# Optimization experiments

Hardware: AMD Instinct MI355X
Metric: run time of the kernel (lower is better)

Reference implementation:

```python
import jax, jax.numpy as jnp
import numpy as np

H, DH, L, G = 4, 16, 6, 256


def _ln(x, eps=1e-6):
    m = x.mean(-1, keepdims=True)
    v = ((x - m) ** 2).mean(-1, keepdims=True)
    return (x - m) * jax.lax.rsqrt(v + eps)


def _sh(u):
    # real spherical harmonics l=0,1,2, 'component' normalization (e3nn style), unit input
    x, y, z = u[:, 0], u[:, 1], u[:, 2]
    s3, s15, s5 = 3.0 ** 0.5, 15.0 ** 0.5, 5.0 ** 0.5
    return jnp.stack([
        jnp.ones_like(x),
        s3 * x, s3 * y, s3 * z,
        s15 * x * y, s15 * y * z, (s5 / 2.0) * (3.0 * z * z - 1.0),
        s15 * x * z, (s15 / 2.0) * (x * x - y * y),
    ], axis=-1)


def _seg_softmax(logits, seg, n):
    m = jax.ops.segment_max(logits, seg, num_segments=n)
    ex = jnp.exp(logits - m[seg])
    s = jax.ops.segment_sum(ex, seg, num_segments=n)
    return ex / (s[seg] + 1e-9)


def setup_inputs() -> dict:
    key = jax.random.key(0)
    ks = jax.random.split(key, 24)
    N, E = 16384, 262144
    D = H * DH  # 64

    def w(k, shape, fan_in):
        return (jax.random.normal(k, shape, dtype=jnp.float32) / np.sqrt(fan_in)).astype(jnp.float32)

    inp = {
        'node_num': N,
        'edge_src': jax.random.randint(ks[0], (E,), 0, N, dtype=jnp.int32),
        'edge_dst': jax.random.randint(ks[1], (E,), 0, N, dtype=jnp.int32),
        'edge_vec': jax.random.normal(ks[2], (E, 3), dtype=jnp.float32) * 2.0,
        'batch': jnp.sort(jax.random.randint(ks[3], (N,), 0, G, dtype=jnp.int32)),
        'node_atom': jax.random.randint(ks[4], (N,), 0, 120, dtype=jnp.int32),
        'ele_embed_w': jax.random.normal(ks[5], (120, 32), dtype=jnp.float32) * 0.05,
        'W_embed': w(ks[6], (32, D), 32),
        'W_edge': w(ks[7], (32 + 32 + 9 + 64, D), 137),
        'Wq': w(ks[8], (L, D, D), D),
        'Wk': w(ks[9], (L, D, D), D),
        'Wv': w(ks[10], (L, D, D), D),
        'Wr1': w(ks[11], (L, 64, 64), 64),
        'Wr2': w(ks[12], (L, 64, H), 64),
        'Wo': w(ks[13], (L, D, D), D),
        'W1': w(ks[14], (L, D, 4 * D), D),
        'W2': w(ks[15], (L, 4 * D, D), 4 * D),
        'W_feat': w(ks[16], (D, 512), D),
        'hW1': w(ks[17], (512, 64), 512),
        'hb1': jnp.zeros((64,), jnp.float32),
        'hW2': w(ks[18], (64, 64), 64),
        'hb2': jnp.zeros((64,), jnp.float32),
        'hW3': w(ks[19], (64, 1), 64),
        'hb3': jnp.zeros((1,), jnp.float32),
    }
    return inp


def reference(node_num, edge_src, edge_dst, edge_vec, batch, node_atom,
              ele_embed_w, W_embed, W_edge, Wq, Wk, Wv, Wr1, Wr2, Wo, W1, W2,
              W_feat, hW1, hb1, hW2, hb2, hW3, hb3):
    N = int(node_num)
    E = edge_src.shape[0]

    # edge geometry: SH of permuted+normalized edge vector, gaussian RBF of length
    r = jnp.linalg.norm(edge_vec, axis=1)
    u = edge_vec[:, jnp.array([1, 2, 0])] / (r[:, None] + 1e-12)
    sh = _sh(u)                                   # [E, 9]
    centers = jnp.linspace(0.0, 10.0, 64, dtype=jnp.float32)
    width = 0.5 * 10.0 / 64.0
    rbf = jnp.exp(-((r[:, None] - centers) ** 2) / (2.0 * width * width))  # [E, 64]
    mask = r < 10.0                               # range_dis = [0, 10)

    # w2v path: atom embedding, edge features = cat(src, dst)
    nf = ele_embed_w[node_atom]                   # [N, 32]
    x = nf @ W_embed                              # [N, 64]
    e_ctx = jnp.concatenate([nf[edge_src], nf[edge_dst], sh, rbf], axis=-1)  # [E,137]
    e = e_ctx @ W_edge                            # [E, 64]

    for l in range(L):
        h = _ln(x)
        q = (h[edge_dst] @ Wq[l]).reshape(E, H, DH)
        src_in = h[edge_src] + e
        k = (src_in @ Wk[l]).reshape(E, H, DH)
        v = (src_in @ Wv[l]).reshape(E, H, DH)
        radial = jax.nn.silu(rbf @ Wr1[l]) @ Wr2[l]           # [E, H]
        logits = (q * k).sum(-1) / np.sqrt(DH) + radial        # [E, H]
        logits = jnp.where(mask[:, None], logits, -1e9)
        alpha = _seg_softmax(logits, edge_dst, N)              # softmax over in-edges
        msg = (alpha[..., None] * v).reshape(E, H * DH)
        agg = jax.ops.segment_sum(msg, edge_dst, num_segments=N)
        x = x + agg @ Wo[l]
        h2 = _ln(x)
        x = x + jax.nn.silu(h2 @ W1[l]) @ W2[l]

    feat = _ln(x @ W_feat)                        # [N, 512], irreps_feature = 512x0e
    hh = jax.nn.relu(_ln(feat @ hW1 + hb1))
    hh = jax.nn.relu(_ln(hh @ hW2 + hb2))
    energy = hh @ hW3 + hb3                       # [N, 1]
    pooled = jax.ops.segment_sum(energy, batch, num_segments=G) / np.sqrt(72.0)
    return pooled
```

## Files before the change

### kernel.cpp

```cpp
#include <hip/hip_runtime.h>

typedef short s8v __attribute__((ext_vector_type(8)));
typedef float f32x4 __attribute__((ext_vector_type(4)));
typedef unsigned short u16;

__device__ __forceinline__ float bf2f(u16 h){
  union { unsigned u; float f; } v; v.u = ((unsigned)h) << 16; return v.f;
}
__device__ __forceinline__ u16 f2bf(float f){
  union { float f; unsigned u; } v; v.f = f;
  unsigned u = v.u;
  return (u16)((u + 0x7fffu + ((u >> 16) & 1u)) >> 16);
}
#define MFMA(a,b,c) __builtin_amdgcn_mfma_f32_16x16x32_bf16((a),(b),(c),0,0,0)

#define WREDUCE64(s) { s += __shfl_xor(s,1); s += __shfl_xor(s,2); s += __shfl_xor(s,4); \
                       s += __shfl_xor(s,8); s += __shfl_xor(s,16); s += __shfl_xor(s,32); }
#define QREDUCE16(s) { s += __shfl_xor(s,1); s += __shfl_xor(s,2); s += __shfl_xor(s,4); s += __shfl_xor(s,8); }

__device__ __forceinline__ float quad_butterfly16(float* val, int c){
  float v8[8], v4[4], v2[2];
  #pragma unroll
  for(int t=0;t<8;t++){
    float sent = (c&1) ? val[2*t] : val[2*t+1];
    float got = __shfl_xor(sent, 1);
    v8[t] = ((c&1) ? val[2*t+1] : val[2*t]) + got;
  }
  #pragma unroll
  for(int t=0;t<4;t++){
    float sent = ((c>>1)&1) ? v8[2*t] : v8[2*t+1];
    float got = __shfl_xor(sent, 2);
    v4[t] = (((c>>1)&1) ? v8[2*t+1] : v8[2*t]) + got;
  }
  #pragma unroll
  for(int t=0;t<2;t++){
    float sent = ((c>>2)&1) ? v4[2*t] : v4[2*t+1];
    float got = __shfl_xor(sent, 4);
    v2[t] = (((c>>2)&1) ? v4[2*t+1] : v4[2*t]) + got;
  }
  float sent = ((c>>3)&1) ? v2[0] : v2[1];
  float got = __shfl_xor(sent, 8);
  return (((c>>3)&1) ? v2[1] : v2[0]) + got;
}

__global__ __launch_bounds__(256) void k_prep(const float* ele, const float* W_embed, const float* W_edge,
    const float* Wq, const float* Wk, const float* Wv, const float* Wr1, const float* Wo,
    const float* W1, const float* W2, const float* W_feat, const float* hW1, const float* hW2,
    u16* dst){
  int idx = blockIdx.x*256 + threadIdx.x;
  if(idx >= 405248) return;
  u16 v;
  if(idx < 3840){
    v = f2bf(ele[idx]);
  } else if(idx < 5888){
    int l = idx - 3840;
    int cI = l >> 5, rI = l & 31;
    v = f2bf(W_embed[rI*64 + cI]);
  } else if(idx < 16128){
    int l = idx - 5888;
    int cI = l / 160, rI = l - cI*160;
    v = (rI < 137) ? f2bf(W_edge[rI*64 + cI]) : (u16)0;
  } else if(idx < 139008){
    int l = idx - 16128;
    int which = l / 24576;
    int rem = l - which*24576;
    const float* src = (which==0)?Wq:(which==1)?Wk:(which==2)?Wv:(which==3)?Wr1:Wo;
    int b = rem >> 12;
    int r2 = rem & 4095;
    int cI = r2 >> 6, rI = r2 & 63;
    v = f2bf(src[b*4096 + rI*64 + cI]);
  } else if(idx < 237312){
    int l = idx - 139008;
    int b = l / 16384;
    int rem = l - b*16384;
    int cI = rem >> 6, rI = rem & 63;
    v = f2bf(W1[b*16384 + rI*256 + cI]);
  } else if(idx < 335616){
    int l = idx - 237312;
    int b = l / 16384;
    int rem = l - b*16384;
    int cI = rem >> 8, rI = rem & 255;
    v = f2bf(W2[b*16384 + rI*64 + cI]);
  } else if(idx < 368384){
    int l = idx - 335616;
    int cI = l >> 6, rI = l & 63;
    v = f2bf(W_feat[rI*512 + cI]);
  } else if(idx < 401152){
    int l = idx - 368384;
    int cI = l >> 9, rI = l & 511;
    v = f2bf(hW1[rI*64 + cI]);
  } else {
    int l = idx - 401152;
    int cI = l >> 6, rI = l & 63;
    v = f2bf(hW2[rI*64 + cI]);
  }
  dst[idx] = v;
}

__global__ __launch_bounds__(256) void k_count(const int* dstI, int* deg, int E){
  int tid = blockIdx.x*256 + threadIdx.x;
  if(tid < E) atomicAdd(&deg[dstI[tid]], 1);
}
__global__ __launch_bounds__(1024) void k_scan(const int* deg, int* rowptr, int* cursor, int N){
  __shared__ int wsum[17];
  int tid = threadIdx.x;
  int per = (N + 1023) >> 10;
  int base = tid * per;
  int s = 0;
  for(int i=0;i<per;i++){ int idx = base+i; if(idx < N) s += deg[idx]; }
  int lane = tid & 63, wid = tid >> 6;
  int inc = s;
  for(int d=1; d<64; d<<=1){
    int t = __shfl_up(inc, d);
    if(lane >= d) inc += t;
  }
  if(lane == 63) wsum[wid+1] = inc;
  if(tid == 0) wsum[0] = 0;
  __syncthreads();
  if(tid == 0){ for(int w=1; w<=16; w++) wsum[w] += wsum[w-1]; }
  __syncthreads();
  int run = inc - s + wsum[wid];
  for(int i=0;i<per;i++){
    int idx = base + i;
    if(idx < N){ rowptr[idx] = run; cursor[idx] = run; run += deg[idx]; }
  }
  if(tid == 1023) rowptr[N] = wsum[16];
}
__global__ __launch_bounds__(256) void k_scatter(const int* dstI, int* cursor, int* csr, int E){
  int tid = blockIdx.x*256 + threadIdx.x;
  if(tid < E){
    int p = atomicAdd(&cursor[dstI[tid]], 1);
    csr[p] = tid;
  }
}

__global__ __launch_bounds__(256) void k_edge_embed(const int* csr, const int* srcI, const int* dstI,
    const int* atom, const u16* ele, const float* evec, const u16* Bt,
    u16* ebf, float* r2, int* src2, int* dst2, int E){
  int wave = (blockIdx.x*blockDim.x + threadIdx.x) >> 6;
  int lane = threadIdx.x & 63;
  int row0 = wave*16; if(row0 >= E) return;
  int c = lane & 15, q = lane >> 4;
  int p = row0 + c;
  int e = csr[p];
  int sn = srcI[e], dn = dstI[e];
  float vx = evec[(size_t)e*3+0];
  float vy = evec[(size_t)e*3+1];
  float vz = evec[(size_t)e*3+2];
  float r = sqrtf(vx*vx + vy*vy + vz*vz);
  if(q == 0){ r2[p] = r; src2[p] = sn; dst2[p] = dn; }
  float inv = 1.f/(r + 1e-12f);
  float x = vy*inv, y = vz*inv, z = vx*inv;
  const float s3 = 1.7320508075688772f, s15 = 3.872983346207417f;
  const float s5h = 1.118033988749895f, s15h = 1.9364916731037085f;
  float sh[9];
  sh[0] = 1.f; sh[1] = s3*x; sh[2] = s3*y; sh[3] = s3*z;
  sh[4] = s15*x*y; sh[5] = s15*y*z; sh[6] = s5h*(3.f*z*z - 1.f);
  sh[7] = s15*x*z; sh[8] = s15h*(x*x - y*y);
  s8v a[5];
  a[0] = *reinterpret_cast<const s8v*>(ele + (size_t)atom[sn]*32 + q*8);
  a[1] = *reinterpret_cast<const s8v*>(ele + (size_t)atom[dn]*32 + q*8);
  #pragma unroll
  for(int j=0;j<8;j++){
    int col = 64 + q*8 + j;
    u16 v;
    if(q == 0)            v = f2bf(sh[j]);
    else if(col < 73)     v = f2bf(sh[8]);
    else { float d = r - (10.f/63.f)*(float)(col-73); v = f2bf(__expf(-81.92f*d*d)); }
    a[2][j] = (short)v;
  }
  #pragma unroll
  for(int j=0;j<8;j++){
    float d = r - (10.f/63.f)*(float)(23 + q*8 + j);
    a[3][j] = (short)f2bf(__expf(-81.92f*d*d));
  }
  #pragma unroll
  for(int j=0;j<8;j++){
    int col = 128 + q*8 + j;
    u16 v = 0;
    if(col < 137){ float d = r - (10.f/63.f)*(float)(col-73); v = f2bf(__expf(-81.92f*d*d)); }
    a[4][j] = (short)v;
  }
  #pragma unroll
  for(int ct=0; ct<4; ct++){
    f32x4 acc = {0.f,0.f,0.f,0.f};
    #pragma unroll
    for(int kc=0; kc<5; kc++){
      s8v b = *reinterpret_cast<const s8v*>(Bt + (ct*16+c)*160 + kc*32 + q*8);
      acc = MFMA(a[kc], b, acc);
    }
    #pragma unroll
    for(int r_=0;r_<4;r_++) ebf[(size_t)(row0+q*4+r_)*64 + ct*16 + c] = f2bf(acc[r_]);
  }
}

__global__ __launch_bounds__(256) void k_radial6(const float* r2, const u16* Wr1T, const float* Wr2,
    float* rad6, int E){
  int wave = (blockIdx.x*256 + threadIdx.x) >> 6;
  int lane = threadIdx.x & 63;
  int row0 = wave*16; if(row0 >= E) return;
  int c = lane & 15, q = lane >> 4;
  float re = r2[row0 + c];
  s8v r0, r1;
  #pragma unroll
  for(int j=0;j<8;j++){
    float d0 = re - (10.f/63.f)*(float)(q*8+j);
    float d1 = re - (10.f/63.f)*(float)(32+q*8+j);
    r0[j] = (short)f2bf(__expf(-81.92f*d0*d0));
    r1[j] = (short)f2bf(__expf(-81.92f*d1*d1));
  }
  for(int l=0; l<6; l++){
    const u16* W1l = Wr1T + l*4096;
    const float4* wr2v = reinterpret_cast<const float4*>(Wr2 + l*256);
    float val[16];
    #pragma unroll
    for(int i=0;i<16;i++) val[i] = 0.f;
    #pragma unroll
    for(int ct=0; ct<4; ct++){
      s8v bw0 = *reinterpret_cast<const s8v*>(W1l + (ct*16+c)*64 + q*8);
      s8v bw1 = *reinterpret_cast<const s8v*>(W1l + (ct*16+c)*64 + 32 + q*8);
      f32x4 hacc = {0.f,0.f,0.f,0.f};
      hacc = MFMA(r0, bw0, hacc); hacc = MFMA(r1, bw1, hacc);
      float4 w2 = wr2v[ct*16 + c];
      #pragma unroll
      for(int r=0;r<4;r++){
        float y = hacc[r];
        float sv = y / (1.f + __expf(-y));
        val[r*4+0] += sv * w2.x;
        val[r*4+1] += sv * w2.y;
        val[r*4+2] += sv * w2.z;
        val[r*4+3] += sv * w2.w;
      }
    }
    float fin = quad_butterfly16(val, c);
    rad6[(size_t)l*E*4 + (size_t)row0*4 + lane] = fin;
  }
}

__global__ __launch_bounds__(256) void k_pre(const int* atom, const u16* ele, const u16* WembT,
    const u16* WqT0, float* xb, u16* hbf, float* Qt, int M){
  __shared__ u16 ldsH[4][16*72];
  int widL = threadIdx.x >> 6;
  int wave = (blockIdx.x*256 + threadIdx.x) >> 6;
  int lane = threadIdx.x & 63;
  int row0 = wave*16; if(row0 >= M) return;
  int c = lane & 15, q = lane >> 4;
  u16* LH = ldsH[widL];
  int at = atom[row0 + c];
  s8v a = *reinterpret_cast<const s8v*>(ele + (size_t)at*32 + q*8);
  float nx[4][4];
  #pragma unroll
  for(int ct=0; ct<4; ct++){
    s8v b = *reinterpret_cast<const s8v*>(WembT + (ct*16+c)*32 + q*8);
    f32x4 acc = {0.f,0.f,0.f,0.f};
    acc = MFMA(a, b, acc);
    #pragma unroll
    for(int r=0;r<4;r++){
      xb[(size_t)(row0+q*4+r)*64 + ct*16 + c] = acc[r];
      nx[ct][r] = acc[r];
    }
  }
  #pragma unroll
  for(int r=0;r<4;r++){
    float s = nx[0][r]+nx[1][r]+nx[2][r]+nx[3][r];
    QREDUCE16(s);
    float m = s*(1.f/64.f);
    float vv = 0.f;
    #pragma unroll
    for(int ct=0;ct<4;ct++){ float d = nx[ct][r]-m; vv += d*d; }
    QREDUCE16(vv);
    float rs = rsqrtf(vv*(1.f/64.f) + 1e-6f);
    #pragma unroll
    for(int ct=0;ct<4;ct++){
      u16 hb = f2bf((nx[ct][r]-m)*rs);
      hbf[(size_t)(row0+q*4+r)*64 + ct*16 + c] = hb;
      LH[(q*4+r)*72 + ct*16 + c] = hb;
    }
  }
  s8v h0 = *reinterpret_cast<const s8v*>(LH + c*72 + q*8);
  s8v h1 = *reinterpret_cast<const s8v*>(LH + c*72 + 32 + q*8);
  #pragma unroll
  for(int ct=0; ct<4; ct++){
    s8v b0 = *reinterpret_cast<const s8v*>(WqT0 + (ct*16+c)*64 + q*8);
    s8v b1 = *reinterpret_cast<const s8v*>(WqT0 + (ct*16+c)*64 + 32 + q*8);
    f32x4 acc = {0.f,0.f,0.f,0.f};
    acc = MFMA(h0, b0, acc);
    acc = MFMA(h1, b1, acc);
    #pragma unroll
    for(int r=0;r<4;r++) Qt[(size_t)(row0+q*4+r)*64 + c*4 + ct] = acc[r];
  }
}

__global__ __launch_bounds__(256) void k_kvrad(const u16* hbf, const u16* ebf,
    const int* src2, const int* dst2, const float* Qt, const float* r2, const float* radial,
    const u16* WkT, const u16* WvT, u16* vbf, float* exb, int E){
  int wave = (blockIdx.x*256 + threadIdx.x) >> 6;
  int lane = threadIdx.x & 63;
  int row0 = wave*16;
  int c = lane & 15, q = lane >> 4;
  int sr = src2[row0 + c];
  s8v a0, a1;
  {
    s8v h0 = *reinterpret_cast<const s8v*>(hbf + (size_t)sr*64 + q*8);
    s8v h1 = *reinterpret_cast<const s8v*>(hbf + (size_t)sr*64 + 32 + q*8);
    s8v e0 = *reinterpret_cast<const s8v*>(ebf + (size_t)(row0+c)*64 + q*8);
    s8v e1 = *reinterpret_cast<const s8v*>(ebf + (size_t)(row0+c)*64 + 32 + q*8);
    #pragma unroll
    for(int j=0;j<8;j++){
      a0[j] = (short)f2bf(bf2f((u16)h0[j]) + bf2f((u16)e0[j]));
      a1[j] = (short)f2bf(bf2f((u16)h1[j]) + bf2f((u16)e1[j]));
    }
  }
  const float4* QtV = reinterpret_cast<const float4*>(Qt);
  float4 qv[4];
  #pragma unroll
  for(int r=0;r<4;r++){
    int dr = dst2[row0 + q*4 + r];
    qv[r] = QtV[(size_t)dr*16 + c];
  }
  float val[16];
  #pragma unroll
  for(int i=0;i<16;i++) val[i] = 0.f;
  #pragma unroll
  for(int ct=0; ct<4; ct++){
    s8v bk0 = *reinterpret_cast<const s8v*>(WkT + (ct*16+c)*64 + q*8);
    s8v bk1 = *reinterpret_cast<const s8v*>(WkT + (ct*16+c)*64 + 32 + q*8);
    s8v bv0 = *reinterpret_cast<const s8v*>(WvT + (ct*16+c)*64 + q*8);
    s8v bv1 = *reinterpret_cast<const s8v*>(WvT + (ct*16+c)*64 + 32 + q*8);
    f32x4 kacc = {0.f,0.f,0.f,0.f};
    kacc = MFMA(a0, bk0, kacc); kacc = MFMA(a1, bk1, kacc);
    f32x4 vacc = {0.f,0.f,0.f,0.f};
    vacc = MFMA(a0, bv0, vacc); vacc = MFMA(a1, bv1, vacc);
    #pragma unroll
    for(int r=0;r<4;r++){
      vbf[(size_t)row0*64 + (r*4+ct)*64 + q*16 + c] = f2bf(vacc[r]);
      float qc = (ct==0)?qv[r].x:(ct==1)?qv[r].y:(ct==2)?qv[r].z:qv[r].w;
      val[r*4+ct] += 0.25f * kacc[r] * qc;
    }
  }
  float qk = quad_butterfly16(val, c);
  float logit = qk + radial[(size_t)row0*4 + lane];
  int row = row0 + q*4 + (c>>2);
  exb[(size_t)row0*4 + lane] = (r2[row] < 10.f) ? __expf(logit) : 0.f;
}

__global__ __launch_bounds__(256) void k_agg(const int* rowptr, const float* exb, const u16* vbf, u16* aggbf, int N){
  int wave = (blockIdx.x*256 + threadIdx.x) >> 6;
  int lane = threadIdx.x & 63;
  if(wave >= N) return;
  int s0 = rowptr[wave], s1 = rowptr[wave+1];
  float s[4] = {0.f,0.f,0.f,0.f};
  for(int p = s0 + lane; p < s1; p += 64){
    float4 ev = *reinterpret_cast<const float4*>(exb + (size_t)p*4);
    s[0] += ev.x; s[1] += ev.y; s[2] += ev.z; s[3] += ev.w;
  }
  #pragma unroll
  for(int i=0;i<4;i++){ WREDUCE64(s[i]); }
  int ep = lane >> 4, cc = lane & 15;
  int hh = cc >> 2;
  int swz = hh*64 + (cc&3)*4;
  float inv = 1.f/(s[hh] + 1e-9f);
  float a0=0.f, a1=0.f, a2=0.f, a3=0.f;
  for(int p = s0 + ep; p < s1; p += 4){
    int t = p & 15;
    size_t base = (size_t)(p & ~15)*64 + (size_t)((t&3)*256) + (size_t)((t>>2)*16) + swz;
    ushort4 v4 = *reinterpret_cast<const ushort4*>(vbf + base);
    float ex = exb[(size_t)p*4 + hh];
    a0 += ex*bf2f(v4.x); a1 += ex*bf2f(v4.y); a2 += ex*bf2f(v4.z); a3 += ex*bf2f(v4.w);
  }
  a0 += __shfl_xor(a0,16); a0 += __shfl_xor(a0,32);
  a1 += __shfl_xor(a1,16); a1 += __shfl_xor(a1,32);
  a2 += __shfl_xor(a2,16); a2 += __shfl_xor(a2,32);
  a3 += __shfl_xor(a3,16); a3 += __shfl_xor(a3,32);
  if(ep == 0){
    ushort4 o;
    o.x = f2bf(a0*inv); o.y = f2bf(a1*inv); o.z = f2bf(a2*inv); o.w = f2bf(a3*inv);
    *reinterpret_cast<ushort4*>(aggbf + (size_t)wave*64 + cc*4) = o;
  }
}

__global__ __launch_bounds__(256) void k_mega(const u16* aggbf, const u16* WoT, float* x,
    const u16* W1T, const u16* W2T, const u16* WqTn, float* Qt, u16* hbf, u16* xbf,
    int writex, int haveQ, int M){
  __shared__ u16 ldsH[4][16*72];
  __shared__ u16 ldsT[4][16*264];
  int widL = threadIdx.x >> 6;
  int wave = (blockIdx.x*256 + threadIdx.x) >> 6;
  int lane = threadIdx.x & 63;
  int row0 = wave*16; if(row0 >= M) return;
  int c = lane & 15, q = lane >> 4;
  u16* LH = ldsH[widL];
  u16* LT = ldsT[widL];
  {
    s8v a0 = *reinterpret_cast<const s8v*>(aggbf + (size_t)(row0+c)*64 + q*8);
    s8v a1 = *reinterpret_cast<const s8v*>(aggbf + (size_t)(row0+c)*64 + 32 + q*8);
    float nx[4][4];
    #pragma unroll
    for(int ct=0; ct<4; ct++){
      s8v b0 = *reinterpret_cast<const s8v*>(WoT + (ct*16+c)*64 + q*8);
      s8v b1 = *reinterpret_cast<const s8v*>(WoT + (ct*16+c)*64 + 32 + q*8);
      f32x4 acc = {0.f,0.f,0.f,0.f};
      acc = MFMA(a0, b0, acc);
      acc = MFMA(a1, b1, acc);
      #pragma unroll
      for(int r=0;r<4;r++){
        size_t idx = (size_t)(row0+q*4+r)*64 + ct*16 + c;
        float t = x[idx] + acc[r];
        x[idx] = t;
        nx[ct][r] = t;
      }
    }
    #pragma unroll
    for(int r=0;r<4;r++){
      float s = nx[0][r]+nx[1][r]+nx[2][r]+nx[3][r];
      QREDUCE16(s);
      float m = s*(1.f/64.f);
      float vv = 0.f;
      #pragma unroll
      for(int ct=0;ct<4;ct++){ float d = nx[ct][r]-m; vv += d*d; }
      QREDUCE16(vv);
      float rs = rsqrtf(vv*(1.f/64.f) + 1e-6f);
      #pragma unroll
      for(int ct=0;ct<4;ct++)
        LH[(q*4+r)*72 + ct*16 + c] = f2bf((nx[ct][r]-m)*rs);
    }
  }
  {
    s8v h0 = *reinterpret_cast<const s8v*>(LH + c*72 + q*8);
    s8v h1 = *reinterpret_cast<const s8v*>(LH + c*72 + 32 + q*8);
    #pragma unroll
    for(int ct=0; ct<16; ct++){
      s8v b0 = *reinterpret_cast<const s8v*>(W1T + (ct*16+c)*64 + q*8);
      s8v b1 = *reinterpret_cast<const s8v*>(W1T + (ct*16+c)*64 + 32 + q*8);
      f32x4 acc = {0.f,0.f,0.f,0.f};
      acc = MFMA(h0, b0, acc);
      acc = MFMA(h1, b1, acc);
      #pragma unroll
      for(int r=0;r<4;r++){
        float y = acc[r];
        LT[(q*4+r)*264 + ct*16 + c] = f2bf(y / (1.f + __expf(-y)));
      }
    }
  }
  {
    s8v a[8];
    #pragma unroll
    for(int kc=0; kc<8; kc++)
      a[kc] = *reinterpret_cast<const s8v*>(LT + c*264 + kc*32 + q*8);
    float nx[4][4];
    #pragma unroll
    for(int ct=0; ct<4; ct++){
      f32x4 acc = {0.f,0.f,0.f,0.f};
      #pragma unroll
      for(int kc=0; kc<8; kc++){
        s8v b = *reinterpret_cast<const s8v*>(W2T + (ct*16+c)*256 + kc*32 + q*8);
        acc = MFMA(a[kc], b, acc);
      }
      #pragma unroll
      for(int r=0;r<4;r++){
        size_t idx = (size_t)(row0+q*4+r)*64 + ct*16 + c;
        float t = x[idx] + acc[r];
        x[idx] = t;
        nx[ct][r] = t;
        if(writex) xbf[idx] = f2bf(t);
      }
    }
    #pragma unroll
    for(int r=0;r<4;r++){
      float s = nx[0][r]+nx[1][r]+nx[2][r]+nx[3][r];
      QREDUCE16(s);
      float m = s*(1.f/64.f);
      float vv = 0.f;
      #pragma unroll
      for(int ct=0;ct<4;ct++){ float d = nx[ct][r]-m; vv += d*d; }
      QREDUCE16(vv);
      float rs = rsqrtf(vv*(1.f/64.f) + 1e-6f);
      #pragma unroll
      for(int ct=0;ct<4;ct++){
        u16 hb = f2bf((nx[ct][r]-m)*rs);
        hbf[(size_t)(row0+q*4+r)*64 + ct*16 + c] = hb;
        LH[(q*4+r)*72 + ct*16 + c] = hb;
      }
    }
  }
  if(haveQ){
    s8v h0 = *reinterpret_cast<const s8v*>(LH + c*72 + q*8);
    s8v h1 = *reinterpret_cast<const s8v*>(LH + c*72 + 32 + q*8);
    #pragma unroll
    for(int ct=0; ct<4; ct++){
      s8v b0 = *reinterpret_cast<const s8v*>(WqTn + (ct*16+c)*64 + q*8);
      s8v b1 = *reinterpret_cast<const s8v*>(WqTn + (ct*16+c)*64 + 32 + q*8);
      f32x4 acc = {0.f,0.f,0.f,0.f};
      acc = MFMA(h0, b0, acc);
      acc = MFMA(h1, b1, acc);
      #pragma unroll
      for(int r=0;r<4;r++) Qt[(size_t)(row0+q*4+r)*64 + c*4 + ct] = acc[r];
    }
  }
}

__global__ __launch_bounds__(256) void k_feat_ln(const u16* A, const u16* Bt, u16* out, int M){
  int wave = (blockIdx.x*256 + threadIdx.x) >> 6;
  int lane = threadIdx.x & 63;
  int row0 = wave*16; if(row0 >= M) return;
  int c = lane & 15, q = lane >> 4;
  s8v a0 = *reinterpret_cast<const s8v*>(A + (size_t)(row0+c)*64 + q*8);
  s8v a1 = *reinterpret_cast<const s8v*>(A + (size_t)(row0+c)*64 + 32 + q*8);
  float fa[32][4];
  #pragma unroll
  for(int ct=0; ct<32; ct++){
    s8v b0 = *reinterpret_cast<const s8v*>(Bt + (ct*16+c)*64 + q*8);
    s8v b1 = *reinterpret_cast<const s8v*>(Bt + (ct*16+c)*64 + 32 + q*8);
    f32x4 acc = {0.f,0.f,0.f,0.f};
    acc = MFMA(a0, b0, acc);
    acc = MFMA(a1, b1, acc);
    #pragma unroll
    for(int r=0;r<4;r++) fa[ct][r] = acc[r];
  }
  #pragma unroll
  for(int r=0;r<4;r++){
    float s = 0.f;
    #pragma unroll
    for(int ct=0;ct<32;ct++) s += fa[ct][r];
    QREDUCE16(s);
    float m = s*(1.f/512.f);
    float vv = 0.f;
    #pragma unroll
    for(int ct=0;ct<32;ct++){ float d = fa[ct][r]-m; vv += d*d; }
    QREDUCE16(vv);
    float rs = rsqrtf(vv*(1.f/512.f) + 1e-6f);
    #pragma unroll
    for(int ct=0;ct<32;ct++)
      out[(size_t)(row0+q*4+r)*512 + ct*16 + c] = f2bf((fa[ct][r]-m)*rs);
  }
}

__global__ __launch_bounds__(256) void k_head1_ln(const u16* A, const u16* Bt, const float* hb, u16* out, int M){
  int wave = (blockIdx.x*256 + threadIdx.x) >> 6;
  int lane = threadIdx.x & 63;
  int row0 = wave*16; if(row0 >= M) return;
  int c = lane & 15, q = lane >> 4;
  s8v a[16];
  #pragma unroll
  for(int kc=0; kc<16; kc++)
    a[kc] = *reinterpret_cast<const s8v*>(A + (size_t)(row0+c)*512 + kc*32 + q*8);
  float y[4][4];
  #pragma unroll
  for(int ct=0; ct<4; ct++){
    f32x4 acc = {0.f,0.f,0.f,0.f};
    #pragma unroll
    for(int kc=0; kc<16; kc++){
      s8v b = *reinterpret_cast<const s8v*>(Bt + (size_t)(ct*16+c)*512 + kc*32 + q*8);
      acc = MFMA(a[kc], b, acc);
    }
    float bi = hb[ct*16+c];
    #pragma unroll
    for(int r=0;r<4;r++) y[ct][r] = acc[r] + bi;
  }
  #pragma unroll
  for(int r=0;r<4;r++){
    float s = y[0][r]+y[1][r]+y[2][r]+y[3][r];
    QREDUCE16(s);
    float m = s*(1.f/64.f);
    float vv = 0.f;
    #pragma unroll
    for(int ct=0;ct<4;ct++){ float d = y[ct][r]-m; vv += d*d; }
    QREDUCE16(vv);
    float rs = rsqrtf(vv*(1.f/64.f) + 1e-6f);
    #pragma unroll
    for(int ct=0;ct<4;ct++)
      out[(size_t)(row0+q*4+r)*64 + ct*16 + c] = f2bf(fmaxf((y[ct][r]-m)*rs, 0.f));
  }
}

__global__ __launch_bounds__(256) void k_head2_energy(const u16* A, const u16* Bt, const float* hb,
    const float* hW3, const float* hb3, const int* batch, float* pooled, int M){
  int wave = (blockIdx.x*256 + threadIdx.x) >> 6;
  int lane = threadIdx.x & 63;
  int row0 = wave*16; if(row0 >= M) return;
  int c = lane & 15, q = lane >> 4;
  s8v a0 = *reinterpret_cast<const s8v*>(A + (size_t)(row0+c)*64 + q*8);
  s8v a1 = *reinterpret_cast<const s8v*>(A + (size_t)(row0+c)*64 + 32 + q*8);
  float y[4][4];
  #pragma unroll
  for(int ct=0; ct<4; ct++){
    s8v b0 = *reinterpret_cast<const s8v*>(Bt + (ct*16+c)*64 + q*8);
    s8v b1 = *reinterpret_cast<const s8v*>(Bt + (ct*16+c)*64 + 32 + q*8);
    f32x4 acc = {0.f,0.f,0.f,0.f};
    acc = MFMA(a0, b0, acc);
    acc = MFMA(a1, b1, acc);
    float bi = hb[ct*16+c];
    #pragma unroll
    for(int r=0;r<4;r++) y[ct][r] = acc[r] + bi;
  }
  float w3[4];
  #pragma unroll
  for(int ct=0;ct<4;ct++) w3[ct] = hW3[ct*16+c];
  float ep[4];
  #pragma unroll
  for(int r=0;r<4;r++){
    float s = y[0][r]+y[1][r]+y[2][r]+y[3][r];
    QREDUCE16(s);
    float m = s*(1.f/64.f);
    float vv = 0.f;
    #pragma unroll
    for(int ct=0;ct<4;ct++){ float d = y[ct][r]-m; vv += d*d; }
    QREDUCE16(vv);
    float rs = rsqrtf(vv*(1.f/64.f) + 1e-6f);
    float e = 0.f;
    #pragma unroll
    for(int ct=0;ct<4;ct++) e += fmaxf((y[ct][r]-m)*rs, 0.f) * w3[ct];
    QREDUCE16(e);
    ep[r] = e;
  }
  if(c < 4){
    float ev = (c==0)?ep[0]:(c==1)?ep[1]:(c==2)?ep[2]:ep[3];
    int row = row0 + q*4 + c;
    atomicAdd(&pooled[batch[row]], ev + hb3[0]);
  }
}

__global__ __launch_bounds__(256) void k_out(const float* pooled, float* out, int G){
  int tid = blockIdx.x*256 + threadIdx.x;
  if(tid < G) out[tid] = pooled[tid] * 0.11785113019775793f;
}

extern "C" void kernel_launch(void* const* d_in, const int* in_sizes, int n_in,
                              void* d_out, int out_size, void* d_ws, size_t ws_size,
                              hipStream_t stream){
  const int*   edge_src  = (const int*)d_in[1];
  const int*   edge_dst  = (const int*)d_in[2];
  const float* edge_vec  = (const float*)d_in[3];
  const int*   batch     = (const int*)d_in[4];
  const int*   node_atom = (const int*)d_in[5];
  const float* ele    = (const float*)d_in[6];
  const float* W_embed= (const float*)d_in[7];
  const float* W_edge = (const float*)d_in[8];
  const float* Wq = (const float*)d_in[9];
  const float* Wk = (const float*)d_in[10];
  const float* Wv = (const float*)d_in[11];
  const float* Wr1= (const float*)d_in[12];
  const float* Wr2= (const float*)d_in[13];
  const float* Wo = (const float*)d_in[14];
  const float* W1 = (const float*)d_in[15];
  const float* W2 = (const float*)d_in[16];
  const float* W_feat=(const float*)d_in[17];
  const float* hW1= (const float*)d_in[18];
  const float* hb1= (const float*)d_in[19];
  const float* hW2= (const float*)d_in[20];
  const float* hb2= (const float*)d_in[21];
  const float* hW3= (const float*)d_in[22];
  const float* hb3= (const float*)d_in[23];
  (void)n_in; (void)ws_size;

  const int E = in_sizes[1];
  const int N = in_sizes[4];
  const int G = out_size;

  char* base = (char*)d_ws;
  size_t off = 0;
  #define ALLOC(ty, name, count) ty* name = (ty*)(base + off); off = (off + (size_t)(count)*sizeof(ty) + 255) & ~(size_t)255;
  ALLOC(float, r2,    E)
  ALLOC(int,   src2,  E)
  ALLOC(int,   dst2,  E)
  ALLOC(u16,   ebf,   (size_t)E*64)
  ALLOC(u16,   vbf,   (size_t)E*64)
  ALLOC(float, exb,   (size_t)E*4)
  ALLOC(float, rad6,  (size_t)E*4*6)
  ALLOC(u16,   hbf,   (size_t)N*64)
  ALLOC(u16,   aggbf, (size_t)N*64)
  ALLOC(u16,   xbf,   (size_t)N*64)
  ALLOC(float, Qt,    (size_t)N*64)
  ALLOC(float, xb,    (size_t)N*64)
  ALLOC(int,   deg,   N)
  ALLOC(int,   rowptr,N+1)
  ALLOC(int,   cursor,N)
  ALLOC(int,   csr,   E)
  ALLOC(float, pooled,G)
  ALLOC(u16, ele_bf, 120*32)
  ALLOC(u16, WembT, 64*32)
  ALLOC(u16, WedgeT,64*160)
  ALLOC(u16, WqT,  6*64*64)
  ALLOC(u16, WkT,  6*64*64)
  ALLOC(u16, WvT,  6*64*64)
  ALLOC(u16, Wr1T, 6*64*64)
  ALLOC(u16, WoT,  6*64*64)
  ALLOC(u16, W1T,  6*256*64)
  ALLOC(u16, W2T,  6*64*256)
  ALLOC(u16, WfT,  512*64)
  ALLOC(u16, hW1T, 64*512)
  ALLOC(u16, hW2T, 64*64)
  #undef ALLOC
  u16* featbf = ebf;
  u16* hh1    = (u16*)exb;

  auto cdiv = [](int a, int b){ return (a + b - 1)/b; };

  k_prep<<<cdiv(405248,256),256,0,stream>>>(ele, W_embed, W_edge, Wq, Wk, Wv, Wr1, Wo,
                                            W1, W2, W_feat, hW1, hW2, ele_bf);

  hipMemsetAsync(deg, 0, (size_t)N*sizeof(int), stream);
  hipMemsetAsync(pooled, 0, (size_t)G*sizeof(float), stream);

  k_count<<<cdiv(E,256),256,0,stream>>>(edge_dst, deg, E);
  k_scan<<<1,1024,0,stream>>>(deg, rowptr, cursor, N);
  k_scatter<<<cdiv(E,256),256,0,stream>>>(edge_dst, cursor, csr, E);
  k_edge_embed<<<E/64, 256, 0, stream>>>(csr, edge_src, edge_dst, node_atom, ele_bf, edge_vec,
                                         WedgeT, ebf, r2, src2, dst2, E);
  k_radial6<<<E/64,256,0,stream>>>(r2, Wr1T, Wr2, rad6, E);
  k_pre<<<N/64,256,0,stream>>>(node_atom, ele_bf, WembT, WqT, xb, hbf, Qt, N);

  for(int l=0; l<6; l++){
    k_kvrad<<<E/64,256,0,stream>>>(hbf, ebf, src2, dst2, Qt, r2, rad6 + (size_t)l*E*4,
                                   WkT + l*4096, WvT + l*4096, vbf, exb, E);
    k_agg<<<cdiv(N,4),256,0,stream>>>(rowptr, exb, vbf, aggbf, N);
    k_mega<<<N/64,256,0,stream>>>(aggbf, WoT + l*4096, xb,
                                  W1T + l*16384, W2T + l*16384,
                                  WqT + ((l<5)?(l+1):0)*4096, Qt, hbf, xbf,
                                  (l==5)?1:0, (l<5)?1:0, N);
  }

  k_feat_ln<<<N/64,256,0,stream>>>(xbf, WfT, featbf, N);
  k_head1_ln<<<N/64,256,0,stream>>>(featbf, hW1T, hb1, hh1, N);
  k_head2_energy<<<N/64,256,0,stream>>>(hh1, hW2T, hb2, hW3, hb3, batch, pooled, N);
  k_out<<<cdiv(G,256),256,0,stream>>>(pooled, (float*)d_out, G);
}
```

Measured before the change: 816.0 us.

## Replace per-edge radial MLP with interpolated lookup table over distance

The radial MLP depends only on the edge distance, so it is tabulated once per layer on a fine uniform grid over [0,10]. k_kvrad then linearly interpolates from the table instead of reading a precomputed per-edge, per-layer radial array. This removes the large rad6 buffer writes and reads and the per-edge MFMA work, at the cost of a small interpolation error. Block barriers are also added in the MLP kernel around shared-memory reuse.

```diff
diff --git a/kernel.cpp b/kernel.cpp
--- a/kernel.cpp
+++ b/kernel.cpp
@@ -194,13 +194,14 @@
   }
 }
 
-__global__ __launch_bounds__(256) void k_radial6(const float* r2, const u16* Wr1T, const float* Wr2,
-    float* rad6, int E){
+#define RG 4096
+#define RGROWS 4112
+__global__ __launch_bounds__(256) void k_radtab(const u16* Wr1T, const float* Wr2, float* radtab){
   int wave = (blockIdx.x*256 + threadIdx.x) >> 6;
   int lane = threadIdx.x & 63;
-  int row0 = wave*16; if(row0 >= E) return;
+  int row0 = wave*16; if(row0 >= RGROWS) return;
   int c = lane & 15, q = lane >> 4;
-  float re = r2[row0 + c];
+  float re = (10.f/RG)*(float)(row0 + c);
   s8v r0, r1;
   #pragma unroll
   for(int j=0;j<8;j++){
@@ -233,7 +234,9 @@
       }
     }
     float fin = quad_butterfly16(val, c);
-    rad6[(size_t)l*E*4 + (size_t)row0*4 + lane] = fin;
+    int row = row0 + q*4 + (c>>2);
+    if(row <= RG)
+      radtab[(size_t)l*RGROWS*4 + (size_t)row0*4 + lane] = fin;
   }
 }
 
@@ -292,7 +295,7 @@
 }
 
 __global__ __launch_bounds__(256) void k_kvrad(const u16* hbf, const u16* ebf,
-    const int* src2, const int* dst2, const float* Qt, const float* r2, const float* radial,
+    const int* src2, const int* dst2, const float* Qt, const float* r2, const float* radtab,
     const u16* WkT, const u16* WvT, u16* vbf, float* exb, int E){
   int wave = (blockIdx.x*256 + threadIdx.x) >> 6;
   int lane = threadIdx.x & 63;
@@ -339,9 +342,17 @@
     }
   }
   float qk = quad_butterfly16(val, c);
-  float logit = qk + radial[(size_t)row0*4 + lane];
   int row = row0 + q*4 + (c>>2);
-  exb[(size_t)row0*4 + lane] = (r2[row] < 10.f) ? __expf(logit) : 0.f;
+  float re = r2[row];
+  float t = re * ((float)RG/10.f);
+  t = fminf(fmaxf(t, 0.f), (float)RG - 0.0001f);
+  int i0 = (int)t;
+  float fr = t - (float)i0;
+  int h = c & 3;
+  float lo = radtab[(size_t)i0*4 + h];
+  float hi = radtab[(size_t)(i0+1)*4 + h];
+  float logit = qk + lo + (hi - lo)*fr;
+  exb[(size_t)row0*4 + lane] = (re < 10.f) ? __expf(logit) : 0.f;
 }
 
 __global__ __launch_bounds__(256) void k_agg(const int* rowptr, const float* exb, const u16* vbf, u16* aggbf, int N){
@@ -425,6 +436,7 @@
         LH[(q*4+r)*72 + ct*16 + c] = f2bf((nx[ct][r]-m)*rs);
     }
   }
+  __syncthreads();
   {
     s8v h0 = *reinterpret_cast<const s8v*>(LH + c*72 + q*8);
     s8v h1 = *reinterpret_cast<const s8v*>(LH + c*72 + 32 + q*8);
@@ -442,6 +454,7 @@
       }
     }
   }
+  __syncthreads();
   {
     s8v a[8];
     #pragma unroll
@@ -666,7 +679,7 @@
   ALLOC(u16,   ebf,   (size_t)E*64)
   ALLOC(u16,   vbf,   (size_t)E*64)
   ALLOC(float, exb,   (size_t)E*4)
-  ALLOC(float, rad6,  (size_t)E*4*6)
+  ALLOC(float, radtab,(size_t)6*RGROWS*4)
   ALLOC(u16,   hbf,   (size_t)N*64)
   ALLOC(u16,   aggbf, (size_t)N*64)
   ALLOC(u16,   xbf,   (size_t)N*64)
@@ -707,11 +720,11 @@
   k_scatter<<<cdiv(E,256),256,0,stream>>>(edge_dst, cursor, csr, E);
   k_edge_embed<<<E/64, 256, 0, stream>>>(csr, edge_src, edge_dst, node_atom, ele_bf, edge_vec,
                                          WedgeT, ebf, r2, src2, dst2, E);
-  k_radial6<<<E/64,256,0,stream>>>(r2, Wr1T, Wr2, rad6, E);
+  k_radtab<<<cdiv(RGROWS*4,256),256,0,stream>>>(Wr1T, Wr2, radtab);
   k_pre<<<N/64,256,0,stream>>>(node_atom, ele_bf, WembT, WqT, xb, hbf, Qt, N);
 
   for(int l=0; l<6; l++){
-    k_kvrad<<<E/64,256,0,stream>>>(hbf, ebf, src2, dst2, Qt, r2, rad6 + (size_t)l*E*4,
+    k_kvrad<<<E/64,256,0,stream>>>(hbf, ebf, src2, dst2, Qt, r2, radtab + (size_t)l*RGROWS*4,
                                    WkT + l*4096, WvT + l*4096, vbf, exb, E);
     k_agg<<<cdiv(N,4),256,0,stream>>>(rowptr, exb, vbf, aggbf, N);
     k_mega<<<N/64,256,0,stream>>>(aggbf, WoT + l*4096, xb,
```

Result: faster. 748.7 us (-8.2%).
